# Optimization experiments

Measured on AMD Instinct MI355X. Metric: run time of the kernel, lower is better.

## Reference

```python
import jax, jax.numpy as jnp
import numpy as np

NEG_INF = -1e30


def setup_inputs() -> dict:
    key = jax.random.key(0)
    kx, km, kq, kk, kv, ko = jax.random.split(key, 6)
    B, D, L = 2, 1024, 2048
    H, DK = 16, 64
    x = jax.random.normal(kx, (B, D, L), dtype=jnp.float32)
    mask = (jax.random.uniform(km, (B, L)) < 0.9).astype(jnp.float32)
    # per-head projection weights, stacked: (H, D, DK); output proj (D, H*DK)==(D, D)
    sq = 1.0 / np.sqrt(D)
    Wq = jax.random.normal(kq, (H, D, DK), dtype=jnp.float32) * sq
    Wk = jax.random.normal(kk, (H, D, DK), dtype=jnp.float32) * sq
    Wv = jax.random.normal(kv, (H, D, DK), dtype=jnp.float32) * sq
    Wo = jax.random.normal(ko, (D, H * DK), dtype=jnp.float32) * sq
    return {"x": x, "mask": mask, "Wq": Wq, "Wk": Wk, "Wv": Wv, "Wo": Wo}


def reference(x, mask, Wq, Wk, Wv, Wo):
    # x: (B, D, L); original transposes to (B, L, D)
    B, D, L = x.shape
    H, _, DK = Wq.shape
    xt = jnp.transpose(x, (0, 2, 1))  # (B, L, D)
    q = jnp.einsum('bld,hdk->bhlk', xt, Wq)
    k = jnp.einsum('bld,hdk->bhlk', xt, Wk)
    v = jnp.einsum('bld,hdk->bhlk', xt, Wv)
    scores = jnp.einsum('bhlk,bhmk->bhlm', q, k) * (1.0 / np.sqrt(DK))
    # masked log-softmax over keys (hmask), squad-style: mask*logit + (1-mask)*-1e30
    hmask = mask[:, None, None, :]  # (B,1,1,Lk)
    masked = hmask * scores + (1.0 - hmask) * NEG_INF
    logp = jax.nn.log_softmax(masked, axis=-1)
    # second softmax over the log-probs, then multiplicative vmask on query dim
    p = jax.nn.softmax(logp, axis=-1) * mask[:, None, :, None]
    heads = jnp.einsum('bhlm,bhmk->bhlk', p, v)  # (B,H,L,DK)
    head = jnp.transpose(heads, (0, 2, 1, 3)).reshape(B, L, H * DK)
    out = jnp.einsum('ble,de->bld', head, Wo)  # matmul(head, Wo) with Wo (D, H*DK)... 
    # NOTE: torch.matmul(head, Wo) treats Wo as (H*DK_in, D_out) only if square; here
    # Wo is (D, H*DK) with D == H*DK, and torch contracts head's last dim with Wo's FIRST dim:
    out = head @ Wo  # (B, L, H*DK) @ (D, H*DK) requires D==H*DK; contracts dim 0 of Wo
    return jnp.transpose(out, (0, 2, 1))  # (B, D, L)


if __name__ == "__main__":
    print(reference(**setup_inputs()).shape)
```

## Files before the change

### kernel.cpp

```cpp
#include <hip/hip_runtime.h>
#include <hip/hip_bf16.h>

typedef unsigned short u16;
typedef unsigned int u32;
typedef unsigned long long u64;
typedef short s8v __attribute__((ext_vector_type(8)));
typedef short s4v __attribute__((ext_vector_type(4)));
typedef __bf16 bfv8 __attribute__((ext_vector_type(8)));
typedef float f4 __attribute__((ext_vector_type(4)));

static constexpr int B = 2, D = 1024, L = 2048, H = 16, DK = 64, E = 1024;
static constexpr float QSCALE = 0.125f * 1.44269504088896340736f;
static constexpr float SMB = -16.0f;
static constexpr float MASKB = -12000.0f;

#define DEV __device__ __forceinline__

DEV u16 f2bf(float f) {
  unsigned int u = __float_as_uint(f);
  u += 0x7FFFu + ((u >> 16) & 1u);
  return (u16)(u >> 16);
}
DEV float fexp2(float x) { return __builtin_amdgcn_exp2f(x); }
DEV u32 pkbf(float a, float b) {
  __hip_bfloat162 h = __float22bfloat162_rn(float2{a, b});
  u32 r;
  __builtin_memcpy(&r, &h, 4);
  return r;
}
DEV bfv8 cat8(s4v a, s4v b) {
  s8v r;
#pragma unroll
  for (int i = 0; i < 4; ++i) {
    r[i] = a[i];
    r[i + 4] = b[i];
  }
  return __builtin_bit_cast(bfv8, r);
}
DEV int kperm(int kk) {
  return (kk & 96) | (((kk >> 2) & 3) << 3) | (((kk >> 4) & 1) << 2) |
         (kk & 3);
}

#define GLD_LDS16(gp, lp)                                                     \
  __builtin_amdgcn_global_load_lds(                                           \
      (const __attribute__((address_space(1))) void*)(gp),                    \
      (__attribute__((address_space(3))) void*)(lp), 16, 0, 0)

__global__ __launch_bounds__(256) void k_prep(
    const float* __restrict__ x, const float* __restrict__ Wq,
    const float* __restrict__ Wk, const float* __restrict__ Wv,
    const float* __restrict__ Wo, u16* __restrict__ xt, u16* __restrict__ Wt,
    u16* __restrict__ WoT) {
  __shared__ u16 t[64][67];
  const int tid = threadIdx.x;
  const int g = blockIdx.x;
  const float* src;
  u16* dst;
  int sld, dld;
  if (g < 1024) {
    const int b = g >> 9, dt = (g >> 5) & 15, lt = g & 31;
    src = x + ((size_t)b * D + dt * 64) * L + lt * 64;
    sld = L;
    dst = xt + ((size_t)b * L + lt * 64) * D + dt * 64;
    dld = D;
  } else if (g < 1792) {
    const int u = g - 1024;
    const int w = u >> 8, h = (u >> 4) & 15, dt = u & 15;
    const float* Ws = (w == 0) ? Wq : ((w == 1) ? Wk : Wv);
    src = Ws + ((size_t)h * D + dt * 64) * DK;
    sld = DK;
    dst = Wt + ((size_t)(w * H + h) * DK) * D + dt * 64;
    dld = D;
  } else {
    const int v = g - 1792;
    const int et = v >> 4, dt = v & 15;
    src = Wo + ((size_t)et * 64) * D + dt * 64;
    sld = D;
    dst = WoT + ((size_t)dt * 64) * E + et * 64;
    dld = E;
  }
  const int r = tid >> 2, c16 = (tid & 3) * 16;
#pragma unroll
  for (int j = 0; j < 16; j += 4) {
    const f4 v4 = *(const f4*)(src + (size_t)r * sld + c16 + j);
    t[r][c16 + j]     = f2bf(v4[0]);
    t[r][c16 + j + 1] = f2bf(v4[1]);
    t[r][c16 + j + 2] = f2bf(v4[2]);
    t[r][c16 + j + 3] = f2bf(v4[3]);
  }
  __syncthreads();
  s8v o0, o1;
#pragma unroll
  for (int i = 0; i < 8; ++i) {
    o0[i] = (short)t[c16 + i][r];
    o1[i] = (short)t[c16 + 8 + i][r];
  }
  *(s8v*)(dst + (size_t)r * dld + c16)     = o0;
  *(s8v*)(dst + (size_t)r * dld + c16 + 8) = o1;
}

template <int AR, int BR>
DEV void gemm_tile(const u16* __restrict__ A, const u16* __restrict__ Bt,
                   int arow0, int brow0, u16* As, u16* Bs,
                   f4 (&acc)[AR / 32][BR / 32]) {
  const int tid = threadIdx.x;
  const int wid = tid >> 6, lane = tid & 63;
  const int q = lane >> 4, ln = lane & 15;
  const int wr = wid >> 1, wc = wid & 1;
  const int lrow = lane >> 3;
  const int lc = (lane & 7) ^ lrow;
  const int f0 = (q ^ (ln & 7)) * 8;
  const int f1 = ((q + 4) ^ (ln & 7)) * 8;
  constexpr int MT = AR / 32, NT = BR / 32;

  for (int k0 = 0; k0 < 1024; k0 += 64) {
    __syncthreads();
#pragma unroll
    for (int j = 0; j < AR / 32; ++j) {
      const int rb = wid * (AR / 4) + j * 8;
      GLD_LDS16(A + (size_t)(arow0 + rb + lrow) * 1024 + k0 + lc * 8,
                As + rb * 64);
    }
#pragma unroll
    for (int j = 0; j < BR / 32; ++j) {
      const int rb = wid * (BR / 4) + j * 8;
      GLD_LDS16(Bt + (size_t)(brow0 + rb + lrow) * 1024 + k0 + lc * 8,
                Bs + rb * 64);
    }
    __syncthreads();
#pragma unroll
    for (int ks = 0; ks < 2; ++ks) {
      const int fc = ks ? f1 : f0;
      bfv8 af[MT], bf[NT];
#pragma unroll
      for (int mt = 0; mt < MT; ++mt)
        af[mt] = *(const bfv8*)(As + (wr * (AR / 2) + mt * 16 + ln) * 64 + fc);
#pragma unroll
      for (int nt = 0; nt < NT; ++nt)
        bf[nt] = *(const bfv8*)(Bs + (wc * (BR / 2) + nt * 16 + ln) * 64 + fc);
#pragma unroll
      for (int mt = 0; mt < MT; ++mt)
#pragma unroll
        for (int nt = 0; nt < NT; ++nt)
          acc[mt][nt] = __builtin_amdgcn_mfma_f32_16x16x32_bf16(
              af[mt], bf[nt], acc[mt][nt], 0, 0, 0);
    }
  }
}

__global__ __launch_bounds__(256, 3) void k_qkvg(
    const u16* __restrict__ xt, const u16* __restrict__ Wt,
    u16* __restrict__ Q, u16* __restrict__ K, u16* __restrict__ Vt) {
  __shared__ u16 As[128 * 64];
  __shared__ u16 Bs[128 * 64];
  const int orig = blockIdx.x;
  const int xcd = orig & 7, kk = orig >> 3;
  const int bm = (xcd >> 1) * 8 + (kk & 7);
  const int bn = (xcd & 1) * 12 + (kk >> 3);
  f4 acc[4][4];
#pragma unroll
  for (int mt = 0; mt < 4; ++mt)
#pragma unroll
    for (int nt = 0; nt < 4; ++nt) acc[mt][nt] = (f4){0.f, 0.f, 0.f, 0.f};
  gemm_tile<128, 128>(xt, Wt, bm * 128, bn * 128, As, Bs, acc);

  const int tid = threadIdx.x, wid = tid >> 6, lane = tid & 63;
  const int q = lane >> 4, ln = lane & 15;
  const int wr = wid >> 1, wc = wid & 1;
  const int h2 = bn * 2 + wc;
  const int wsel = h2 >> 4, h = h2 & 15;
  const int b = bm >> 4;
  const int lbase = (bm & 15) * 128 + wr * 64;
  if (wsel == 0) {
    u16* dst = Q + (size_t)(b * H + h) * L * DK;
#pragma unroll
    for (int mt = 0; mt < 4; ++mt)
#pragma unroll
      for (int nt = 0; nt < 4; ++nt)
#pragma unroll
        for (int r = 0; r < 4; ++r)
          dst[(size_t)(lbase + mt * 16 + q * 4 + r) * DK + nt * 16 + ln] =
              f2bf(acc[mt][nt][r] * QSCALE);
  } else if (wsel == 1) {
    u16* dst = K + (size_t)(b * H + h) * L * DK;
#pragma unroll
    for (int mt = 0; mt < 4; ++mt)
#pragma unroll
      for (int nt = 0; nt < 4; ++nt)
#pragma unroll
        for (int r = 0; r < 4; ++r)
          dst[(size_t)(lbase + mt * 16 + q * 4 + r) * DK + nt * 16 + ln] =
              f2bf(acc[mt][nt][r]);
  } else {
    u16* dst = Vt + (size_t)(b * H + h) * DK * L;
#pragma unroll
    for (int mt = 0; mt < 4; ++mt)
#pragma unroll
      for (int nt = 0; nt < 4; ++nt) {
        const u64 pk = (u64)pkbf(acc[mt][nt][0], acc[mt][nt][1]) |
                       ((u64)pkbf(acc[mt][nt][2], acc[mt][nt][3]) << 32);
        *(u64*)(dst + (size_t)(nt * 16 + ln) * L + lbase + mt * 16 + q * 4) =
            pk;
      }
  }
}

__global__ __launch_bounds__(512, 4) void k_attn(
    const u16* __restrict__ Q, const u16* __restrict__ K,
    const u16* __restrict__ Vt, const float* __restrict__ mask,
    u16* __restrict__ Hd) {
  __shared__ u16 kt[2][128 * 64];
  __shared__ u16 vt[2][2][64 * 64];
  __shared__ __align__(16) float mb[L];
  const int orig = blockIdx.x;
  const int xcd = orig & 7, kk2 = orig >> 3;
  const int bh = xcd * 4 + (kk2 >> 4);
  const int lt = kk2 & 15;
  const int b = bh >> 4, h = bh & 15;
  const int tid = threadIdx.x;
  const int w = tid >> 6, lane = tid & 63, q = lane >> 4, ln = lane & 15;
  const int wq = w >> 1, wk = w & 1;
  for (int i = tid; i < L; i += 512)
    mb[i] = (mask[(size_t)b * L + i] != 0.0f) ? SMB : MASKB;

  const u16* Qp = Q + (size_t)bh * L * DK;
  const u16* Kp = K + (size_t)bh * L * DK;
  const u16* Vp = Vt + (size_t)bh * DK * L;
  const int lq = lt * 128 + wq * 32;

  bfv8 qf[2][2];
#pragma unroll
  for (int mt = 0; mt < 2; ++mt) {
    qf[mt][0] = *(const bfv8*)(Qp + (size_t)(lq + mt * 16 + ln) * DK + q * 8);
    qf[mt][1] =
        *(const bfv8*)(Qp + (size_t)(lq + mt * 16 + ln) * DK + 32 + q * 8);
  }

  const int lrow = lane >> 3;
  const int lc = (lane & 7) ^ lrow;
  const int c0 = (q ^ (ln & 7)) * 8;
  const int c1 = ((q + 4) ^ (ln & 7)) * 8;
  int kpr[2];
#pragma unroll
  for (int j = 0; j < 2; ++j) kpr[j] = kperm(w * 16 + j * 8 + lrow);

  auto stage = [&](int m0, int bufi) {
#pragma unroll
    for (int j = 0; j < 2; ++j) {
      GLD_LDS16(Kp + (size_t)(m0 + kpr[j]) * DK + lc * 8,
                &kt[bufi][(w * 16 + j * 8) * 64]);
    }
    const int fr = w * 8 + lrow;
#pragma unroll
    for (int kh = 0; kh < 2; ++kh) {
      GLD_LDS16(Vp + (size_t)fr * L + m0 + kh * 64 + lc * 8,
                &vt[bufi][kh][(w * 8) * 64]);
    }
  };

  union {
    f4 v;
    float f[4];
  } ot[2][4];
#pragma unroll
  for (int mt = 0; mt < 2; ++mt)
#pragma unroll
    for (int dt = 0; dt < 4; ++dt) ot[mt][dt].v = (f4){0.f, 0.f, 0.f, 0.f};
  float lp[2] = {0.f, 0.f};

  stage(0, 0);
  for (int it = 0; it < L / 128; ++it) {
    const int m0 = it * 128;
    __syncthreads();
    if (it + 1 < L / 128) stage(m0 + 128, (it + 1) & 1);
    const int cur = it & 1;
    const u16* ktc = &kt[cur][0];
    const u16* vtc = &vt[cur][wk][0];

    s4v pbe[2];
    bfv8 pbx[2][2];
#pragma unroll
    for (int nt = 0; nt < 4; ++nt) {
      const int krow = wk * 64 + nt * 16 + ln;
      const bfv8 kf0 = *(const bfv8*)(ktc + krow * 64 + c0);
      const bfv8 kf1 = *(const bfv8*)(ktc + krow * 64 + c1);
      const f4 mbv = *(const f4*)(mb + m0 + wk * 64 + (nt >> 1) * 32 +
                                  (nt & 1) * 4 + q * 8);
#pragma unroll
      for (int mt = 0; mt < 2; ++mt) {
        f4 a = mbv;
        __builtin_amdgcn_s_setprio(1);
        a = __builtin_amdgcn_mfma_f32_16x16x32_bf16(kf0, qf[mt][0], a, 0, 0,
                                                    0);
        a = __builtin_amdgcn_mfma_f32_16x16x32_bf16(kf1, qf[mt][1], a, 0, 0,
                                                    0);
        __builtin_amdgcn_s_setprio(0);
        const float p0 = fexp2(a[0]);
        const float p1 = fexp2(a[1]);
        const float p2 = fexp2(a[2]);
        const float p3 = fexp2(a[3]);
        lp[mt] += (p0 + p1) + (p2 + p3);
        const u64 pk = (u64)pkbf(p0, p1) | ((u64)pkbf(p2, p3) << 32);
        const s4v pc = __builtin_bit_cast(s4v, pk);
        if (nt & 1)
          pbx[mt][nt >> 1] = cat8(pbe[mt], pc);
        else
          pbe[mt] = pc;
      }
    }
    __builtin_amdgcn_s_setprio(1);
#pragma unroll
    for (int g = 0; g < 2; ++g) {
#pragma unroll
      for (int dt = 0; dt < 4; ++dt) {
        const int vrow = dt * 16 + ln;
        const bfv8 av =
            *(const bfv8*)(vtc + vrow * 64 + (((g * 4 + q) ^ (ln & 7)) * 8));
#pragma unroll
        for (int mt = 0; mt < 2; ++mt)
          ot[mt][dt].v = __builtin_amdgcn_mfma_f32_16x16x32_bf16(
              av, pbx[mt][g], ot[mt][dt].v, 0, 0, 0);
      }
    }
    __builtin_amdgcn_s_setprio(0);
  }
#pragma unroll
  for (int mt = 0; mt < 2; ++mt) {
    lp[mt] += __shfl_xor(lp[mt], 16);
    lp[mt] += __shfl_xor(lp[mt], 32);
  }
  __syncthreads();
  float* sOt = (float*)&kt[0][0];
  float* sLp = (float*)&vt[0][0][0];
  if (wk) {
#pragma unroll
    for (int mt = 0; mt < 2; ++mt) {
#pragma unroll
      for (int dt = 0; dt < 4; ++dt)
        *(f4*)(sOt + ((((wq * 2 + mt) * 4 + dt) * 64) + lane) * 4) =
            ot[mt][dt].v;
      sLp[(wq * 2 + mt) * 64 + lane] = lp[mt];
    }
  }
  __syncthreads();
  if (!wk) {
#pragma unroll
    for (int mt = 0; mt < 2; ++mt) {
#pragma unroll
      for (int dt = 0; dt < 4; ++dt)
        ot[mt][dt].v +=
            *(const f4*)(sOt + ((((wq * 2 + mt) * 4 + dt) * 64) + lane) * 4);
      lp[mt] += sLp[(wq * 2 + mt) * 64 + lane];
      const float linv =
          (mb[lq + mt * 16 + ln] > -100.0f) ? (1.0f / lp[mt]) : 0.0f;
#pragma unroll
      for (int dt = 0; dt < 4; ++dt) {
        const u64 pk =
            (u64)pkbf(ot[mt][dt].f[0] * linv, ot[mt][dt].f[1] * linv) |
            ((u64)pkbf(ot[mt][dt].f[2] * linv, ot[mt][dt].f[3] * linv) << 32);
        *(u64*)(Hd + (size_t)(b * L + lq + mt * 16 + ln) * E + h * DK +
                dt * 16 + q * 4) = pk;
      }
    }
  }
}

__global__ __launch_bounds__(256, 4) void k_projg(const u16* __restrict__ WoT,
                                                  const u16* __restrict__ Hd,
                                                  float* __restrict__ out) {
  __shared__ u16 As[64 * 64];
  __shared__ u16 Bs[64 * 64];
  const int orig = blockIdx.x;
  const int xcd = orig & 7, kk = orig >> 3;
  const int bm = kk & 15;
  const int bn = xcd * 8 + (kk >> 4);
  f4 acc[2][2];
#pragma unroll
  for (int mt = 0; mt < 2; ++mt)
#pragma unroll
    for (int nt = 0; nt < 2; ++nt) acc[mt][nt] = (f4){0.f, 0.f, 0.f, 0.f};
  gemm_tile<64, 64>(WoT, Hd, bm * 64, bn * 64, As, Bs, acc);

  const int tid = threadIdx.x, wid = tid >> 6, lane = tid & 63;
  const int q = lane >> 4, ln = lane & 15;
  const int wr = wid >> 1, wc = wid & 1;
#pragma unroll
  for (int mt = 0; mt < 2; ++mt)
#pragma unroll
    for (int nt = 0; nt < 2; ++nt)
#pragma unroll
      for (int r = 0; r < 4; ++r) {
        const int d = bm * 64 + wr * 32 + mt * 16 + q * 4 + r;
        const int n = bn * 64 + wc * 32 + nt * 16 + ln;
        const int bb = n >> 11, l = n & 2047;
        out[((size_t)(bb * D + d)) * L + l] = acc[mt][nt][r];
      }
}

extern "C" void kernel_launch(void* const* d_in, const int* in_sizes, int n_in,
                              void* d_out, int out_size, void* d_ws,
                              size_t ws_size, hipStream_t stream) {
  const float* x    = (const float*)d_in[0];
  const float* mask = (const float*)d_in[1];
  const float* Wq   = (const float*)d_in[2];
  const float* Wk   = (const float*)d_in[3];
  const float* Wv   = (const float*)d_in[4];
  const float* Wo   = (const float*)d_in[5];
  u16* ws = (u16*)d_ws;
  u16* Qws  = ws;
  u16* Kws  = ws + 4194304;
  u16* Vtws = ws + 8388608;
  u16* WoTw = ws + 12582912;
  u16* Wtws = ws + 13631488;
  u16* xtws = ws + 16777216;
  u16* Hdws = ws + 16777216;

  k_prep<<<2048, 256, 0, stream>>>(x, Wq, Wk, Wv, Wo, xtws, Wtws, WoTw);
  k_qkvg<<<768, 256, 0, stream>>>(xtws, Wtws, Qws, Kws, Vtws);
  k_attn<<<512, 512, 0, stream>>>(Qws, Kws, Vtws, mask, Hdws);
  k_projg<<<1024, 256, 0, stream>>>(WoTw, Hdws, (float*)d_out);
}
```

Before: 168.4 us.

## Re-split attention warps into 2 query groups by 4 key groups

Changes the per-block warp layout in the attention kernel from 4 query groups × 2 key halves to 2 query groups of 64 rows × 4 key quarters of 32 columns. Each warp now handles four query tiles, so every K and V fragment loaded from shared memory is reused across more MFMAs. This cuts LDS read traffic per FLOP. In exchange, accumulator register pressure doubles (16 f4 outputs per warp) and the final cross-warp reduction becomes a two-stage tree through shared memory with extra barriers, which may lower occupancy under the launch bound of 4.

```diff
diff --git a/kernel.cpp b/kernel.cpp
--- a/kernel.cpp
+++ b/kernel.cpp
@@ -220,18 +220,18 @@
   const int b = bh >> 4, h = bh & 15;
   const int tid = threadIdx.x;
   const int w = tid >> 6, lane = tid & 63, q = lane >> 4, ln = lane & 15;
-  const int wq = w >> 1, wk = w & 1;
+  const int wq = w >> 2, wk = w & 3;
   for (int i = tid; i < L; i += 512)
     mb[i] = (mask[(size_t)b * L + i] != 0.0f) ? SMB : MASKB;
 
   const u16* Qp = Q + (size_t)bh * L * DK;
   const u16* Kp = K + (size_t)bh * L * DK;
   const u16* Vp = Vt + (size_t)bh * DK * L;
-  const int lq = lt * 128 + wq * 32;
-
-  bfv8 qf[2][2];
-#pragma unroll
-  for (int mt = 0; mt < 2; ++mt) {
+  const int lq = lt * 128 + wq * 64;
+
+  bfv8 qf[4][2];
+#pragma unroll
+  for (int mt = 0; mt < 4; ++mt) {
     qf[mt][0] = *(const bfv8*)(Qp + (size_t)(lq + mt * 16 + ln) * DK + q * 8);
     qf[mt][1] =
         *(const bfv8*)(Qp + (size_t)(lq + mt * 16 + ln) * DK + 32 + q * 8);
@@ -259,15 +259,12 @@
     }
   };
 
-  union {
-    f4 v;
-    float f[4];
-  } ot[2][4];
-#pragma unroll
-  for (int mt = 0; mt < 2; ++mt)
-#pragma unroll
-    for (int dt = 0; dt < 4; ++dt) ot[mt][dt].v = (f4){0.f, 0.f, 0.f, 0.f};
-  float lp[2] = {0.f, 0.f};
+  f4 ot[4][4];
+#pragma unroll
+  for (int mt = 0; mt < 4; ++mt)
+#pragma unroll
+    for (int dt = 0; dt < 4; ++dt) ot[mt][dt] = (f4){0.f, 0.f, 0.f, 0.f};
+  float lp[4] = {0.f, 0.f, 0.f, 0.f};
 
   stage(0, 0);
   for (int it = 0; it < L / 128; ++it) {
@@ -276,19 +273,18 @@
     if (it + 1 < L / 128) stage(m0 + 128, (it + 1) & 1);
     const int cur = it & 1;
     const u16* ktc = &kt[cur][0];
-    const u16* vtc = &vt[cur][wk][0];
-
-    s4v pbe[2];
-    bfv8 pbx[2][2];
-#pragma unroll
-    for (int nt = 0; nt < 4; ++nt) {
-      const int krow = wk * 64 + nt * 16 + ln;
+    const u16* vtc = &vt[cur][wk >> 1][0];
+
+    s4v pbe[4];
+    bfv8 pbx[4];
+#pragma unroll
+    for (int nt = 0; nt < 2; ++nt) {
+      const int krow = wk * 32 + nt * 16 + ln;
       const bfv8 kf0 = *(const bfv8*)(ktc + krow * 64 + c0);
       const bfv8 kf1 = *(const bfv8*)(ktc + krow * 64 + c1);
-      const f4 mbv = *(const f4*)(mb + m0 + wk * 64 + (nt >> 1) * 32 +
-                                  (nt & 1) * 4 + q * 8);
-#pragma unroll
-      for (int mt = 0; mt < 2; ++mt) {
+      const f4 mbv = *(const f4*)(mb + m0 + wk * 32 + nt * 4 + q * 8);
+#pragma unroll
+      for (int mt = 0; mt < 4; ++mt) {
         f4 a = mbv;
         __builtin_amdgcn_s_setprio(1);
         a = __builtin_amdgcn_mfma_f32_16x16x32_bf16(kf0, qf[mt][0], a, 0, 0,
@@ -303,62 +299,98 @@
         lp[mt] += (p0 + p1) + (p2 + p3);
         const u64 pk = (u64)pkbf(p0, p1) | ((u64)pkbf(p2, p3) << 32);
         const s4v pc = __builtin_bit_cast(s4v, pk);
-        if (nt & 1)
-          pbx[mt][nt >> 1] = cat8(pbe[mt], pc);
+        if (nt)
+          pbx[mt] = cat8(pbe[mt], pc);
         else
           pbe[mt] = pc;
       }
     }
+    const int cb = (((wk & 1) * 4 + q) ^ (ln & 7)) * 8;
     __builtin_amdgcn_s_setprio(1);
 #pragma unroll
-    for (int g = 0; g < 2; ++g) {
-#pragma unroll
-      for (int dt = 0; dt < 4; ++dt) {
-        const int vrow = dt * 16 + ln;
-        const bfv8 av =
-            *(const bfv8*)(vtc + vrow * 64 + (((g * 4 + q) ^ (ln & 7)) * 8));
-#pragma unroll
-        for (int mt = 0; mt < 2; ++mt)
-          ot[mt][dt].v = __builtin_amdgcn_mfma_f32_16x16x32_bf16(
-              av, pbx[mt][g], ot[mt][dt].v, 0, 0, 0);
-      }
+    for (int dt = 0; dt < 4; ++dt) {
+      const int vrow = dt * 16 + ln;
+      const bfv8 av = *(const bfv8*)(vtc + vrow * 64 + cb);
+#pragma unroll
+      for (int mt = 0; mt < 4; ++mt)
+        ot[mt][dt] = __builtin_amdgcn_mfma_f32_16x16x32_bf16(av, pbx[mt],
+                                                             ot[mt][dt], 0,
+                                                             0, 0);
     }
     __builtin_amdgcn_s_setprio(0);
   }
 #pragma unroll
-  for (int mt = 0; mt < 2; ++mt) {
+  for (int mt = 0; mt < 4; ++mt) {
     lp[mt] += __shfl_xor(lp[mt], 16);
     lp[mt] += __shfl_xor(lp[mt], 32);
   }
+  float* sA = (float*)&kt[0][0];
+  float* sB = (float*)&vt[0][0][0];
+  float* sL = mb;
   __syncthreads();
-  float* sOt = (float*)&kt[0][0];
-  float* sLp = (float*)&vt[0][0][0];
-  if (wk) {
-#pragma unroll
-    for (int mt = 0; mt < 2; ++mt) {
-#pragma unroll
-      for (int dt = 0; dt < 4; ++dt)
-        *(f4*)(sOt + ((((wq * 2 + mt) * 4 + dt) * 64) + lane) * 4) =
-            ot[mt][dt].v;
-      sLp[(wq * 2 + mt) * 64 + lane] = lp[mt];
-    }
+  if (wk == 1) {
+#pragma unroll
+    for (int mt = 0; mt < 4; ++mt)
+#pragma unroll
+      for (int dt = 0; dt < 4; ++dt)
+        *(f4*)(sA + (((wq * 4 + mt) * 4 + dt) * 64 + lane) * 4) = ot[mt][dt];
+  }
+  if (wk == 3) {
+#pragma unroll
+    for (int mt = 0; mt < 4; ++mt)
+#pragma unroll
+      for (int dt = 0; dt < 4; ++dt)
+        *(f4*)(sB + (((wq * 4 + mt) * 4 + dt) * 64 + lane) * 4) = ot[mt][dt];
+  }
+  if (wk != 0 && q == 0) {
+#pragma unroll
+    for (int mt = 0; mt < 4; ++mt)
+      sL[(((wk - 1) * 2 + wq) * 4 + mt) * 16 + ln] = lp[mt];
   }
   __syncthreads();
-  if (!wk) {
-#pragma unroll
-    for (int mt = 0; mt < 2; ++mt) {
-#pragma unroll
-      for (int dt = 0; dt < 4; ++dt)
-        ot[mt][dt].v +=
-            *(const f4*)(sOt + ((((wq * 2 + mt) * 4 + dt) * 64) + lane) * 4);
-      lp[mt] += sLp[(wq * 2 + mt) * 64 + lane];
-      const float linv =
-          (mb[lq + mt * 16 + ln] > -100.0f) ? (1.0f / lp[mt]) : 0.0f;
+  if (wk == 0) {
+#pragma unroll
+    for (int mt = 0; mt < 4; ++mt) {
+#pragma unroll
+      for (int dt = 0; dt < 4; ++dt)
+        ot[mt][dt] +=
+            *(const f4*)(sA + (((wq * 4 + mt) * 4 + dt) * 64 + lane) * 4);
+      lp[mt] += sL[((0 * 2 + wq) * 4 + mt) * 16 + ln] +
+                sL[((1 * 2 + wq) * 4 + mt) * 16 + ln] +
+                sL[((2 * 2 + wq) * 4 + mt) * 16 + ln];
+    }
+  }
+  if (wk == 2) {
+#pragma unroll
+    for (int mt = 0; mt < 4; ++mt)
+#pragma unroll
+      for (int dt = 0; dt < 4; ++dt)
+        ot[mt][dt] +=
+            *(const f4*)(sB + (((wq * 4 + mt) * 4 + dt) * 64 + lane) * 4);
+  }
+  __syncthreads();
+  if (wk == 2) {
+#pragma unroll
+    for (int mt = 0; mt < 4; ++mt)
+#pragma unroll
+      for (int dt = 0; dt < 4; ++dt)
+        *(f4*)(sA + (((wq * 4 + mt) * 4 + dt) * 64 + lane) * 4) = ot[mt][dt];
+  }
+  __syncthreads();
+  if (wk == 0) {
+#pragma unroll
+    for (int mt = 0; mt < 4; ++mt) {
+#pragma unroll
+      for (int dt = 0; dt < 4; ++dt)
+        ot[mt][dt] +=
+            *(const f4*)(sA + (((wq * 4 + mt) * 4 + dt) * 64 + lane) * 4);
+      const float mv = mask[(size_t)b * L + lq + mt * 16 + ln];
+      const float linv = (mv != 0.0f) ? (1.0f / lp[mt]) : 0.0f;
 #pragma unroll
       for (int dt = 0; dt < 4; ++dt) {
         const u64 pk =
-            (u64)pkbf(ot[mt][dt].f[0] * linv, ot[mt][dt].f[1] * linv) |
-            ((u64)pkbf(ot[mt][dt].f[2] * linv, ot[mt][dt].f[3] * linv) << 32);
+            (u64)pkbf(ot[mt][dt][0] * linv, ot[mt][dt][1] * linv) |
+            ((u64)pkbf(ot[mt][dt][2] * linv, ot[mt][dt][3] * linv) << 32);
         *(u64*)(Hd + (size_t)(b * L + lq + mt * 16 + ln) * E + h * DK +
                 dt * 16 + q * 4) = pk;
       }
```

Measured after the change: 315.5 us. +87.4%, slower.
